# Kernel optimization log

Hardware: AMD Instinct MI355X
Metric: run time of the kernel (lower is better)

The kernel has to match this reference:

```python
import jax, jax.numpy as jnp
import numpy as np

BOS_ID = 0
EOS_ID = 1


def setup_inputs() -> dict:
    key = jax.random.key(0)
    ks = jax.random.split(key, 16)
    B, L, F = 64, 200, 512
    H, E, A = 512, 512, 512
    V, T = 50257, 21
    D = E + F  # rnn input_dim
    s = lambda n: 1.0 / np.sqrt(n)
    ref = jax.random.randint(ks[0], (B, T), 2, V, dtype=jnp.int32)
    ref = ref.at[:, 0].set(BOS_ID).at[:, -1].set(EOS_ID)
    return {
        "encoder_output": jax.random.normal(ks[1], (B, L, F), jnp.float32),
        "decoder_init_hidden": jax.random.normal(ks[2], (1, B, H), jnp.float32),
        "encoding_mask": jnp.ones((B, L, 1), jnp.float32),
        "temp_seg": jax.random.uniform(ks[3], (B, 2), jnp.float32),
        "embed_table": jax.random.normal(ks[4], (V, E), jnp.float32) * 0.02,
        "W_ih": jax.random.normal(ks[5], (3 * H, D), jnp.float32) * s(D),
        "W_hh": jax.random.normal(ks[6], (3 * H, H), jnp.float32) * s(H),
        "b_ih": jnp.zeros((3 * H,), jnp.float32),
        "b_hh": jnp.zeros((3 * H,), jnp.float32),
        "Wa_enc": jax.random.normal(ks[7], (F, A), jnp.float32) * s(F),
        "Wa_h": jax.random.normal(ks[8], (H, A), jnp.float32) * s(H),
        "v_att": jax.random.normal(ks[9], (A,), jnp.float32) * s(A),
        "W_out": jax.random.normal(ks[10], (V, H), jnp.float32) * s(H),
        "b_out": jnp.zeros((V,), jnp.float32),
        "ref_caption": ref,
    }


def reference(encoder_output, decoder_init_hidden, encoding_mask, temp_seg,
              embed_table, W_ih, W_hh, b_ih, b_hh,
              Wa_enc, Wa_h, v_att, W_out, b_out, ref_caption):
    # Teacher-forced training forward of RNNSeqDecoder (GRU, 1 layer).
    B, T = ref_caption.shape
    V = embed_table.shape[0]
    enc_proj = jnp.einsum('blf,fa->bla', encoder_output, Wa_enc)  # precompute attn enc term
    mask = encoding_mask[..., 0]  # (B,L)
    h0 = decoder_init_hidden[0]   # (B,H)

    def step(h, word):
        emb = embed_table[word]                                        # (B,E)
        # additive attention over encoder states (masked)
        score = jnp.einsum('bla,a->bl', jnp.tanh(enc_proj + (h @ Wa_h)[:, None, :]), v_att)
        score = jnp.where(mask > 0, score, -1e9)
        attn = jax.nn.softmax(score, axis=1)
        ctx = jnp.einsum('bl,blf->bf', attn, encoder_output)           # (B,F)
        x = jnp.concatenate([emb, ctx], axis=1)                        # (B,E+F)
        # PyTorch GRU cell
        gi = x @ W_ih.T + b_ih
        gh = h @ W_hh.T + b_hh
        i_r, i_z, i_n = jnp.split(gi, 3, axis=1)
        h_r, h_z, h_n = jnp.split(gh, 3, axis=1)
        r = jax.nn.sigmoid(i_r + h_r)
        z = jax.nn.sigmoid(i_z + h_z)
        n = jnp.tanh(i_n + r * h_n)
        h_new = (1.0 - z) * n + z * h
        logp = jax.nn.log_softmax(h_new @ W_out.T + b_out, axis=1)     # (B,V)
        return h_new, logp

    _, logps = jax.lax.scan(step, h0, ref_caption[:, :-1].T)           # (T-1,B,V)
    first = jnp.zeros((B, 1, V), logps.dtype)  # BOS_ID == 0, matches torch.zeros(...) + BOS_ID
    caption_prob = jnp.concatenate([first, jnp.swapaxes(logps, 0, 1)], axis=1)  # (B,T,V)
    return caption_prob
```

## Files before the change

kernel.cpp:

```cpp
#include <hip/hip_runtime.h>
#include <stdint.h>
#include <stddef.h>

#define B_ 64
#define L_ 200
#define F_ 512
#define H_ 512
#define A_ 512
#define E_ 512
#define V_ 50257
#define PADV 50304
#define T_ 21
#define D_ 1024
#define NBLK_LOG 786
#define BH (B_ * H_)
#define BD (B_ * D_)
#define NROW 1280

typedef __attribute__((ext_vector_type(8))) short short8;
typedef __attribute__((ext_vector_type(4))) float f32x4;

__device__ __forceinline__ unsigned short f2b(float f) {
  unsigned int u = __builtin_bit_cast(unsigned int, f);
  u += 0x7FFFu + ((u >> 16) & 1u);
  return (unsigned short)(u >> 16);
}
__device__ __forceinline__ float b2f(unsigned short s) {
  unsigned int u = ((unsigned int)s) << 16;
  return __builtin_bit_cast(float, u);
}
__device__ __forceinline__ f32x4 mfma16(short8 a, short8 b, f32x4 c) {
  return __builtin_amdgcn_mfma_f32_16x16x32_bf16(a, b, c, 0, 0, 0);
}
__device__ __forceinline__ int hsoff(int b, int j) {
  return (((b >> 4) * 16 + (j >> 5)) * 64 + (((j >> 3) & 3) * 16 + (b & 15))) * 8 + (j & 7);
}
__device__ __forceinline__ int xoff(int b, int k) {
  return (((b >> 4) * 32 + (k >> 5)) * 64 + (((k >> 3) & 3) * 16 + (b & 15))) * 8 + (k & 7);
}


__global__ void k_cvt(const float* __restrict__ src, unsigned short* __restrict__ dst, int n4) {
  int i = blockIdx.x * blockDim.x + threadIdx.x;
  int stride = gridDim.x * blockDim.x;
  const float4* s4 = (const float4*)src;
  ushort4* d4 = (ushort4*)dst;
  for (; i < n4; i += stride) {
    float4 v = s4[i];
    ushort4 o;
    o.x = f2b(v.x); o.y = f2b(v.y); o.z = f2b(v.z); o.w = f2b(v.w);
    d4[i] = o;
  }
}

__global__ void k_wfrag(const float* __restrict__ src, unsigned short* __restrict__ dst, int K) {
  int rt = blockIdx.x;
  int r15 = threadIdx.x & 15;
  int row = rt * 16 + r15;
  int nch = K >> 3;
  int kpw = K >> 5;
  for (int kc = threadIdx.x >> 4; kc < nch; kc += 16) {
    const float4* s = (const float4*)(src + (size_t)row * K + kc * 8);
    float4 x = s[0], y = s[1];
    short8 o;
    o[0] = f2b(x.x); o[1] = f2b(x.y); o[2] = f2b(x.z); o[3] = f2b(x.w);
    o[4] = f2b(y.x); o[5] = f2b(y.y); o[6] = f2b(y.z); o[7] = f2b(y.w);
    *(short8*)(dst + ((size_t)(rt * kpw + (kc >> 2)) * 64 + ((kc & 3) * 16 + r15)) * 8) = o;
  }
}

__global__ void k_transcvt(const float* __restrict__ src, unsigned short* __restrict__ dst, int R, int C) {
  __shared__ float tile[64][65];
  int cb = blockIdx.x * 64, rb = blockIdx.y * 64;
  int tx = threadIdx.x & 63, ty = threadIdx.x >> 6;
#pragma unroll
  for (int i = 0; i < 16; ++i) {
    int r = ty * 16 + i;
    tile[r][tx] = src[(size_t)(rb + r) * C + cb + tx];
  }
  __syncthreads();
#pragma unroll
  for (int i = 0; i < 16; ++i) {
    int c = ty * 16 + i;
    dst[(size_t)(cb + c) * R + rb + tx] = f2b(tile[tx][c]);
  }
}

__global__ void k_trans32(const float* __restrict__ src, float* __restrict__ dst, int R, int C) {
  __shared__ float tile[64][65];
  int cb = blockIdx.x * 64, rb = blockIdx.y * 64;
  int tx = threadIdx.x & 63, ty = threadIdx.x >> 6;
#pragma unroll
  for (int i = 0; i < 16; ++i) {
    int r = ty * 16 + i;
    tile[r][tx] = src[(size_t)(rb + r) * C + cb + tx];
  }
  __syncthreads();
#pragma unroll
  for (int i = 0; i < 16; ++i) {
    int c = ty * 16 + i;
    dst[(size_t)(cb + c) * R + rb + tx] = tile[tx][c];
  }
}

__global__ void k_hs0(const float* __restrict__ src, unsigned short* __restrict__ hs) {
  int b = blockIdx.x;
  for (int j = threadIdx.x; j < H_; j += 256)
    hs[hsoff(b, j)] = f2b(src[(size_t)b * H_ + j]);
}

__global__ void k_embAll(const int* __restrict__ ref, const float* __restrict__ et,
                         unsigned short* __restrict__ xAll) {
  int b = blockIdx.x, tp = blockIdx.y;
  int word = ref[b * T_ + tp];
  const float* er = et + (size_t)word * E_;
  unsigned short* dst = xAll + (size_t)tp * BD;
  int c = threadIdx.x;
  const float4* s = (const float4*)(er + c * 8);
  float4 x = s[0], y = s[1];
  short8 o;
  o[0] = f2b(x.x); o[1] = f2b(x.y); o[2] = f2b(x.z); o[3] = f2b(x.w);
  o[4] = f2b(y.x); o[5] = f2b(y.y); o[6] = f2b(y.z); o[7] = f2b(y.w);
  *(short8*)(dst + xoff(b, c * 8)) = o;
}

__global__ __launch_bounds__(256, 2) void k_encproj2(const unsigned short* __restrict__ encb,
                                                     const unsigned short* __restrict__ WaTb,
                                                     unsigned short* __restrict__ epb) {
  __shared__ unsigned short al[32768];
  int tid = threadIdx.x;
  size_t rowbase = (size_t)blockIdx.x * 64;
  for (int idx = tid; idx < 4096; idx += 256) {
    int row = idx >> 6, seg = idx & 63;
    unsigned char* dp = (unsigned char*)al + row * 1024 + ((seg * 16) ^ ((row & 7) << 4));
    *(short8*)dp = *(const short8*)(encb + (rowbase + row) * F_ + seg * 8);
  }
  __syncthreads();
  int w = tid >> 6, lane = tid & 63, ln15 = lane & 15, g = lane >> 4;
  int sw = (ln15 & 7) << 4;
  const unsigned char* alb = (const unsigned char*)al;
  int mrow = w * 16 + ln15;
  for (int nt = 0; nt < 32; ++nt) {
    f32x4 acc = {0.f, 0.f, 0.f, 0.f};
    const unsigned short* brow = WaTb + (size_t)(nt * 16 + ln15) * F_ + 8 * g;
#pragma unroll 4
    for (int kk = 0; kk < 16; ++kk) {
      short8 bf = *(const short8*)(brow + kk * 32);
      short8 af = *(const short8*)(alb + mrow * 1024 + ((kk * 64 + 16 * g) ^ sw));
      acc = mfma16(af, bf, acc);
    }
#pragma unroll
    for (int r = 0; r < 4; ++r) {
      size_t m = rowbase + w * 16 + 4 * g + r;
      epb[m * A_ + nt * 16 + ln15] = f2b(acc[r]);
    }
  }
}

__global__ void k_zero0(float* __restrict__ out) {
  int b = blockIdx.y;
  float* o = out + (size_t)b * T_ * V_;
  int v0 = blockIdx.x * 1024 + threadIdx.x;
#pragma unroll
  for (int i = 0; i < 4; ++i) { int v = v0 + i * 256; if (v < V_) o[v] = 0.f; }
}


__global__ __launch_bounds__(256) void k_hwgh(const unsigned short* __restrict__ Wahf,
                                              const unsigned short* __restrict__ Wfhh,
                                              const unsigned short* __restrict__ hs,
                                              float* __restrict__ hw,
                                              float* __restrict__ ghG) {
  int blk = blockIdx.x;
  int w = threadIdx.x >> 6, lane = threadIdx.x & 63;
  int ln15 = lane & 15, g = lane >> 4;
  if (blk < 32) {
    f32x4 acc = {0.f, 0.f, 0.f, 0.f};
#pragma unroll 4
    for (int kk = 0; kk < 16; ++kk) {
      short8 av = *(const short8*)(Wahf + (((size_t)blk * 16 + kk) * 64 + lane) * 8);
      short8 hv = *(const short8*)(hs + (((size_t)w * 16 + kk) * 64 + lane) * 8);
      acc = mfma16(av, hv, acc);
    }
#pragma unroll
    for (int r = 0; r < 4; ++r) {
      int a = blk * 16 + 4 * g + r;
      int b = w * 16 + ln15;
      hw[(size_t)b * 512 + a] = acc[r];
    }
  } else {
    int base = (blk - 32) * 3;
#pragma unroll
    for (int i = 0; i < 3; ++i) {
      int jt = base + i;
      f32x4 acc = {0.f, 0.f, 0.f, 0.f};
#pragma unroll
      for (int kk = 0; kk < 16; ++kk) {
        short8 wv = *(const short8*)(Wfhh + (((size_t)jt * 16 + kk) * 64 + lane) * 8);
        short8 hv = *(const short8*)(hs + (((size_t)w * 16 + kk) * 64 + lane) * 8);
        acc = mfma16(wv, hv, acc);
      }
#pragma unroll
      for (int r = 0; r < 4; ++r) {
        int j = jt * 16 + 4 * g + r;
        int b = w * 16 + ln15;
        ghG[(size_t)j * B_ + b] = acc[r];
      }
    }
  }
}


__global__ __launch_bounds__(1024) void k_attB(const float* __restrict__ mask,
                                               const float* __restrict__ vatt,
                                               const unsigned short* __restrict__ encb,
                                               const unsigned short* __restrict__ epb,
                                               const float* __restrict__ hw,
                                               unsigned short* __restrict__ xplane) {
  __shared__ float sm[208];
  __shared__ float ctxp[16][F_];
  __shared__ float ctxF[F_];
  int b = blockIdx.x;
  int tid = threadIdx.x;
  int w = tid >> 6, lane = tid & 63;
  float hwv[8], vv[8];
  {
    const float4* hp = (const float4*)(hw + (size_t)b * 512 + lane * 8);
    const float4* vp = (const float4*)(vatt + lane * 8);
    float4 h0 = hp[0], h1 = hp[1], v0 = vp[0], v1 = vp[1];
    hwv[0] = h0.x; hwv[1] = h0.y; hwv[2] = h0.z; hwv[3] = h0.w;
    hwv[4] = h1.x; hwv[5] = h1.y; hwv[6] = h1.z; hwv[7] = h1.w;
    vv[0] = v0.x; vv[1] = v0.y; vv[2] = v0.z; vv[3] = v0.w;
    vv[4] = v1.x; vv[5] = v1.y; vv[6] = v1.z; vv[7] = v1.w;
  }
  for (int l = w; l < L_; l += 16) {
    short8 ev = *(const short8*)(epb + ((size_t)(b * L_ + l)) * 512 + lane * 8);
    float p = 0.f;
#pragma unroll
    for (int j = 0; j < 8; ++j) {
      float x = b2f((unsigned short)ev[j]) + hwv[j];
      float e2 = __expf(x + x);
      p = fmaf(1.f - 2.f / (e2 + 1.f), vv[j], p);
    }
    for (int o = 1; o < 64; o <<= 1) p += __shfl_xor(p, o);
    if (lane == 0) {
      float mk = mask[b * L_ + l];
      sm[l] = (mk > 0.f) ? p : -1e9f;
    }
  }
  __syncthreads();
  if (tid < 64) {
    float m = -1e30f;
    for (int l = tid; l < L_; l += 64) m = fmaxf(m, sm[l]);
    for (int o = 1; o < 64; o <<= 1) m = fmaxf(m, __shfl_xor(m, o));
    float s = 0.f;
    for (int l = tid; l < L_; l += 64) s += __expf(sm[l] - m);
    for (int o = 1; o < 64; o <<= 1) s += __shfl_xor(s, o);
    float inv = 1.f / s;
    for (int l = tid; l < L_; l += 64) sm[l] = __expf(sm[l] - m) * inv;
  }
  __syncthreads();
  float c[8] = {0.f, 0.f, 0.f, 0.f, 0.f, 0.f, 0.f, 0.f};
  for (int l = w; l < L_; l += 16) {
    float wgt = sm[l];
    short8 ev = *(const short8*)(encb + ((size_t)(b * L_ + l)) * 512 + lane * 8);
#pragma unroll
    for (int j = 0; j < 8; ++j) c[j] = fmaf(wgt, b2f((unsigned short)ev[j]), c[j]);
  }
#pragma unroll
  for (int j = 0; j < 8; ++j) ctxp[w][lane * 8 + j] = c[j];
  __syncthreads();
  if (tid < 512) {
    float s = 0.f;
#pragma unroll
    for (int q = 0; q < 16; ++q) s += ctxp[q][tid];
    ctxF[tid] = s;
  }
  __syncthreads();
  if (tid < 64) {
    short8 o;
#pragma unroll
    for (int j = 0; j < 8; ++j) o[j] = f2b(ctxF[tid * 8 + j]);
    *(short8*)(xplane + xoff(b, E_ + tid * 8)) = o;
  }
}


__global__ __launch_bounds__(256) void k_stepB(const unsigned short* __restrict__ Wfih,
                                               const float* __restrict__ bih,
                                               const float* __restrict__ bhh,
                                               const unsigned short* __restrict__ xplane,
                                               const float* __restrict__ ghG,
                                               const float* __restrict__ hBold,
                                               unsigned short* __restrict__ hsnew,
                                               float* __restrict__ hBnew) {
  int bx = blockIdx.x;
  int w = threadIdx.x >> 6, lane = threadIdx.x & 63;
  int ln15 = lane & 15, g = lane >> 4;
  f32x4 z4 = {0.f, 0.f, 0.f, 0.f};
  f32x4 aIr = z4, aIz = z4, aIn = z4;
#pragma unroll 2
  for (int kk = 0; kk < 32; ++kk) {
    short8 xv = *(const short8*)(xplane + (((size_t)w * 32 + kk) * 64 + lane) * 8);
    aIr = mfma16(*(const short8*)(Wfih + (((size_t)(0 * 32 + bx) * 32 + kk) * 64 + lane) * 8), xv, aIr);
    aIz = mfma16(*(const short8*)(Wfih + (((size_t)(32 + bx) * 32 + kk) * 64 + lane) * 8), xv, aIz);
    aIn = mfma16(*(const short8*)(Wfih + (((size_t)(64 + bx) * 32 + kk) * 64 + lane) * 8), xv, aIn);
  }
  int jb = bx * 16;
#pragma unroll
  for (int r = 0; r < 4; ++r) {
    int j = jb + 4 * g + r;
    int b = w * 16 + ln15;
    float ir = aIr[r] + bih[j];
    float iz = aIz[r] + bih[512 + j];
    float in_ = aIn[r] + bih[1024 + j];
    float hrv = ghG[(size_t)j * B_ + b] + bhh[j];
    float hzv = ghG[(size_t)(512 + j) * B_ + b] + bhh[512 + j];
    float hnv = ghG[(size_t)(1024 + j) * B_ + b] + bhh[1024 + j];
    float rg = 1.f / (1.f + __expf(-(ir + hrv)));
    float zg = 1.f / (1.f + __expf(-(iz + hzv)));
    float e2 = __expf(2.f * (in_ + rg * hnv));
    float ng = 1.f - 2.f / (e2 + 1.f);
    float ho = hBold[(size_t)b * H_ + j];
    float hv = (1.f - zg) * ng + zg * ho;
    hBnew[(size_t)b * H_ + j] = hv;
    hsnew[hsoff(b, j)] = f2b(hv);
  }
}


__global__ __launch_bounds__(256) void k_blog(const unsigned short* __restrict__ Wb,
                                              const float* __restrict__ bout,
                                              const unsigned short* __restrict__ hsAll,
                                              float* __restrict__ out,
                                              unsigned short* __restrict__ lws, int mode) {
  __shared__ float tile[2][64][68];
  int tid = threadIdx.x;
  int w = tid >> 6, lane = tid & 63, ln15 = lane & 15, g = lane >> 4;
  int vcol = blockIdx.x * 64 + w * 16 + ln15;
  bool vok = vcol < V_;
  int vr = vok ? vcol : (V_ - 1);
  const unsigned short* brow = Wb + (size_t)vr * H_ + 8 * g;
  short8 wb[16];
#pragma unroll
  for (int kk = 0; kk < 16; ++kk) wb[kk] = *(const short8*)(brow + kk * 32);
  float bo = bout[vr];
  int row = tid >> 2, seg = tid & 3;

  for (int t = 0; t < T_ - 1; ++t) {
    const unsigned short* hp = hsAll + (size_t)(t + 1) * BH;
    int buf = t & 1;
#pragma unroll
    for (int mp = 0; mp < 2; ++mp) {
      f32x4 z4 = {0.f, 0.f, 0.f, 0.f};
      f32x4 acc0 = z4, acc1 = z4;
#pragma unroll
      for (int kk = 0; kk < 16; ++kk) {
        short8 a0 = *(const short8*)(hp + (((mp * 2 + 0) * 16 + kk) * 64 + lane) * 8);
        short8 a1 = *(const short8*)(hp + (((mp * 2 + 1) * 16 + kk) * 64 + lane) * 8);
        acc0 = mfma16(a0, wb[kk], acc0);
        acc1 = mfma16(a1, wb[kk], acc1);
      }
#pragma unroll
      for (int r = 0; r < 4; ++r) {
        int bi0 = (mp * 2 + 0) * 16 + 4 * g + r;
        int bi1 = (mp * 2 + 1) * 16 + 4 * g + r;
        tile[buf][bi0][w * 16 + ln15] = vok ? acc0[r] + bo : -1e30f;
        tile[buf][bi1][w * 16 + ln15] = vok ? acc1[r] + bo : -1e30f;
      }
    }
    __syncthreads();
    float v[16];
#pragma unroll
    for (int q = 0; q < 4; ++q) {
      float4 fv = *(const float4*)&tile[buf][row][seg * 16 + q * 4];
      v[q * 4 + 0] = fv.x; v[q * 4 + 1] = fv.y; v[q * 4 + 2] = fv.z; v[q * 4 + 3] = fv.w;
    }
    int cb = blockIdx.x * 64 + seg * 16;
    if (mode == 1) {
      unsigned short* orow = lws + ((size_t)t * 64 + row) * PADV + cb;
      short8 o0, o1;
#pragma unroll
      for (int i = 0; i < 8; ++i) { o0[i] = f2b(v[i]); o1[i] = f2b(v[8 + i]); }
      *(short8*)orow = o0;
      *(short8*)(orow + 8) = o1;
    } else {
      float* orow = out + ((size_t)row * T_ + (t + 1)) * V_ + cb;
      if (cb + 16 <= V_) {
#pragma unroll
        for (int q = 0; q < 4; ++q)
          *(float4*)(orow + q * 4) = make_float4(v[q * 4], v[q * 4 + 1], v[q * 4 + 2], v[q * 4 + 3]);
      } else {
        for (int i = 0; i < 16; ++i)
          if (cb + i < V_) orow[i] = v[i];
      }
    }
  }
}

__global__ __launch_bounds__(256) void k_lsefin(const unsigned short* __restrict__ lws,
                                                float* __restrict__ out) {
  __shared__ float lm[256], ls[256];
  __shared__ float lvs;
  int rho = blockIdx.x;
  int tp = rho >> 6, b = rho & 63;
  const unsigned short* src = lws + (size_t)(tp * 64 + b) * PADV;
  float* o = out + ((size_t)b * T_ + (tp + 1)) * V_;
  int tid = threadIdx.x;
  float m = -1e30f, s = 0.f;
  for (int i = tid; i < PADV / 8; i += 256) {
    short8 sv = *(const short8*)(src + i * 8);
    float x0 = b2f((unsigned short)sv[0]), x1 = b2f((unsigned short)sv[1]);
    float x2 = b2f((unsigned short)sv[2]), x3 = b2f((unsigned short)sv[3]);
    float x4 = b2f((unsigned short)sv[4]), x5 = b2f((unsigned short)sv[5]);
    float x6 = b2f((unsigned short)sv[6]), x7 = b2f((unsigned short)sv[7]);
    float cm = fmaxf(fmaxf(fmaxf(x0, x1), fmaxf(x2, x3)), fmaxf(fmaxf(x4, x5), fmaxf(x6, x7)));
    float cs = __expf(x0 - cm) + __expf(x1 - cm) + __expf(x2 - cm) + __expf(x3 - cm) +
               __expf(x4 - cm) + __expf(x5 - cm) + __expf(x6 - cm) + __expf(x7 - cm);
    float nm = fmaxf(m, cm);
    s = s * __expf(m - nm) + cs * __expf(cm - nm);
    m = nm;
  }
  lm[tid] = m; ls[tid] = s;
  __syncthreads();
  for (int o2 = 128; o2 > 0; o2 >>= 1) {
    if (tid < o2) {
      float m2 = lm[tid + o2], s2 = ls[tid + o2];
      float nm = fmaxf(lm[tid], m2);
      ls[tid] = ls[tid] * __expf(lm[tid] - nm) + s2 * __expf(m2 - nm);
      lm[tid] = nm;
    }
    __syncthreads();
  }
  if (tid == 0) lvs = lm[0] + logf(ls[0]);
  __syncthreads();
  float Lv = lvs;
  for (int i = tid; i < 6282; i += 256) {
    short8 sv = *(const short8*)(src + i * 8);
    float4 v0, v1;
    v0.x = b2f((unsigned short)sv[0]) - Lv; v0.y = b2f((unsigned short)sv[1]) - Lv;
    v0.z = b2f((unsigned short)sv[2]) - Lv; v0.w = b2f((unsigned short)sv[3]) - Lv;
    v1.x = b2f((unsigned short)sv[4]) - Lv; v1.y = b2f((unsigned short)sv[5]) - Lv;
    v1.z = b2f((unsigned short)sv[6]) - Lv; v1.w = b2f((unsigned short)sv[7]) - Lv;
    *(float4*)(o + i * 8) = v0;
    *(float4*)(o + i * 8 + 4) = v1;
  }
  if (tid == 0) o[50256] = b2f(src[50256]) - Lv;
}

__global__ __launch_bounds__(256) void k_lsefin0(float* __restrict__ out) {
  __shared__ float lm[256], ls[256];
  __shared__ float lvs;
  int rho = blockIdx.x;
  int tp = rho >> 6, b = rho & 63;
  float* o = out + ((size_t)b * T_ + (tp + 1)) * V_;
  int tid = threadIdx.x;
  float m = -1e30f, s = 0.f;
  for (int v = tid; v < V_; v += 256) {
    float x = o[v];
    float nm = fmaxf(m, x);
    s = s * __expf(m - nm) + __expf(x - nm);
    m = nm;
  }
  lm[tid] = m; ls[tid] = s;
  __syncthreads();
  for (int o2 = 128; o2 > 0; o2 >>= 1) {
    if (tid < o2) {
      float m2 = lm[tid + o2], s2 = ls[tid + o2];
      float nm = fmaxf(lm[tid], m2);
      ls[tid] = ls[tid] * __expf(lm[tid] - nm) + s2 * __expf(m2 - nm);
      lm[tid] = nm;
    }
    __syncthreads();
  }
  if (tid == 0) lvs = lm[0] + logf(ls[0]);
  __syncthreads();
  float Lv = lvs;
  for (int v = tid; v < V_; v += 256) o[v] -= Lv;
}


extern "C" void kernel_launch(void* const* d_in, const int* in_sizes, int n_in,
                              void* d_out, int out_size, void* d_ws, size_t ws_size,
                              hipStream_t stream) {
  const float* enc   = (const float*)d_in[0];
  const float* dih   = (const float*)d_in[1];
  const float* mask  = (const float*)d_in[2];
  const float* et    = (const float*)d_in[4];
  const float* Wih   = (const float*)d_in[5];
  const float* Whh   = (const float*)d_in[6];
  const float* bih   = (const float*)d_in[7];
  const float* bhh   = (const float*)d_in[8];
  const float* Waenc = (const float*)d_in[9];
  const float* Wah   = (const float*)d_in[10];
  const float* vatt  = (const float*)d_in[11];
  const float* Wout  = (const float*)d_in[12];
  const float* bout  = (const float*)d_in[13];
  const int*   ref   = (const int*)d_in[14];
  float* out = (float*)d_out;

  char* w = (char*)d_ws;
  size_t o = 0;
  unsigned short* Wb    = (unsigned short*)(w + o); o += (size_t)V_ * H_ * 2;
  unsigned short* Wfih  = (unsigned short*)(w + o); o += (size_t)1536 * 1024 * 2;
  unsigned short* Wfhh  = (unsigned short*)(w + o); o += (size_t)1536 * 512 * 2;
  unsigned short* WaTb  = (unsigned short*)(w + o); o += (size_t)512 * 512 * 2;
  unsigned short* Wahf  = (unsigned short*)(w + o); o += (size_t)512 * 512 * 2;
  float* WahT32 = (float*)(w + o); o += (size_t)512 * 512 * 4;
  unsigned short* encb  = (unsigned short*)(w + o); o += (size_t)B_ * L_ * F_ * 2;
  unsigned short* epb   = (unsigned short*)(w + o); o += (size_t)B_ * L_ * A_ * 2;
  unsigned short* xAll  = (unsigned short*)(w + o); o += (size_t)20 * BD * 2;
  unsigned short* hsAll = (unsigned short*)(w + o); o += (size_t)T_ * BH * 2;
  float* hBAll = (float*)(w + o); o += (size_t)T_ * BH * 4;
  float* ghG   = (float*)(w + o); o += (size_t)1536 * B_ * 4;
  float* hw    = (float*)(w + o); o += (size_t)B_ * A_ * 4 + 256;
  unsigned short* lws = (unsigned short*)(w + o);
  size_t need = o + (size_t)NROW * PADV * 2;
  int mode = (ws_size >= need) ? 1 : 0;

  k_cvt<<<4096, 256, 0, stream>>>(Wout, Wb, V_ * H_ / 4);
  k_cvt<<<2048, 256, 0, stream>>>(enc, encb, B_ * L_ * F_ / 4);
  k_wfrag<<<96, 256, 0, stream>>>(Wih, Wfih, 1024);
  k_wfrag<<<96, 256, 0, stream>>>(Whh, Wfhh, 512);
  k_transcvt<<<dim3(8, 8), 256, 0, stream>>>(Waenc, WaTb, 512, 512);
  k_trans32<<<dim3(8, 8), 256, 0, stream>>>(Wah, WahT32, 512, 512);
  k_wfrag<<<32, 256, 0, stream>>>(WahT32, Wahf, 512);
  k_hs0<<<64, 256, 0, stream>>>(dih, hsAll);
  k_embAll<<<dim3(64, 20), 64, 0, stream>>>(ref, et, xAll);
  k_encproj2<<<200, 256, 0, stream>>>(encb, WaTb, epb);
  k_zero0<<<dim3(50, 64), 256, 0, stream>>>(out);

  for (int t = 0; t < T_ - 1; ++t) {
    const float* hB_t = (t == 0) ? dih : (hBAll + (size_t)t * BH);
    float* hB_n = hBAll + (size_t)(t + 1) * BH;
    const unsigned short* hs_t = hsAll + (size_t)t * BH;
    unsigned short* hs_n = hsAll + (size_t)(t + 1) * BH;
    unsigned short* xp = xAll + (size_t)t * BD;
    k_hwgh<<<64, 256, 0, stream>>>(Wahf, Wfhh, hs_t, hw, ghG);
    k_attB<<<64, 1024, 0, stream>>>(mask, vatt, encb, epb, hw, xp);
    k_stepB<<<32, 256, 0, stream>>>(Wfih, bih, bhh, xp, ghG, hB_t, hs_n, hB_n);
  }
  k_blog<<<NBLK_LOG, 256, 0, stream>>>(Wb, bout, hsAll, out, lws, mode);
  if (mode == 1) k_lsefin<<<1280, 256, 0, stream>>>(lws, out);
  else k_lsefin0<<<1280, 256, 0, stream>>>(out);
}
```

Baseline: 1.362 ms.

## Fuse t=0 zeroing into log-softmax finalize, cache row in LDS, raise MFMA priority

The separate kernel that zeroes the BOS time slice is removed. Those 64 rows are now zeroed by 64 extra blocks appended to the log-softmax finalize launch, which saves one kernel launch. The bf16 finalize kernel now runs with 512 threads and keeps each logit row in a ~100KB LDS buffer during the max/sum pass, so the normalize pass reads from LDS instead of re-reading global memory. The large LDS footprint limits occupancy to about one block per CU. The logits GEMM also raises wave priority with s_setprio around its MFMA section.

```diff
diff --git a/kernel.cpp b/kernel.cpp
--- a/kernel.cpp
+++ b/kernel.cpp
@@ -155,14 +155,6 @@
       epb[m * A_ + nt * 16 + ln15] = f2b(acc[r]);
     }
   }
-}
-
-__global__ void k_zero0(float* __restrict__ out) {
-  int b = blockIdx.y;
-  float* o = out + (size_t)b * T_ * V_;
-  int v0 = blockIdx.x * 1024 + threadIdx.x;
-#pragma unroll
-  for (int i = 0; i < 4; ++i) { int v = v0 + i * 256; if (v < V_) o[v] = 0.f; }
 }
 
 
@@ -350,6 +342,7 @@
   for (int t = 0; t < T_ - 1; ++t) {
     const unsigned short* hp = hsAll + (size_t)(t + 1) * BH;
     int buf = t & 1;
+    __builtin_amdgcn_s_setprio(1);
 #pragma unroll
     for (int mp = 0; mp < 2; ++mp) {
       f32x4 z4 = {0.f, 0.f, 0.f, 0.f};
@@ -369,6 +362,7 @@
         tile[buf][bi1][w * 16 + ln15] = vok ? acc1[r] + bo : -1e30f;
       }
     }
+    __builtin_amdgcn_s_setprio(0);
     __syncthreads();
     float v[16];
 #pragma unroll
@@ -398,18 +392,29 @@
   }
 }
 
-__global__ __launch_bounds__(256) void k_lsefin(const unsigned short* __restrict__ lws,
+__global__ __launch_bounds__(512) void k_lsefin(const unsigned short* __restrict__ lws,
                                                 float* __restrict__ out) {
-  __shared__ float lm[256], ls[256];
+  __shared__ unsigned short srow[PADV];
+  __shared__ float lm[512], ls[512];
   __shared__ float lvs;
-  int rho = blockIdx.x;
+  int bid = blockIdx.x;
+  int tid = threadIdx.x;
+  if (bid >= NROW) {
+    int b = bid - NROW;
+    float* o = out + (size_t)b * T_ * V_;
+    float4 z = make_float4(0.f, 0.f, 0.f, 0.f);
+    for (int i = tid; i < 12564; i += 512) *(float4*)(o + i * 4) = z;
+    if (tid == 0) o[50256] = 0.f;
+    return;
+  }
+  int rho = bid;
   int tp = rho >> 6, b = rho & 63;
   const unsigned short* src = lws + (size_t)(tp * 64 + b) * PADV;
   float* o = out + ((size_t)b * T_ + (tp + 1)) * V_;
-  int tid = threadIdx.x;
   float m = -1e30f, s = 0.f;
-  for (int i = tid; i < PADV / 8; i += 256) {
+  for (int i = tid; i < PADV / 8; i += 512) {
     short8 sv = *(const short8*)(src + i * 8);
+    *(short8*)(srow + i * 8) = sv;
     float x0 = b2f((unsigned short)sv[0]), x1 = b2f((unsigned short)sv[1]);
     float x2 = b2f((unsigned short)sv[2]), x3 = b2f((unsigned short)sv[3]);
     float x4 = b2f((unsigned short)sv[4]), x5 = b2f((unsigned short)sv[5]);
@@ -423,7 +428,7 @@
   }
   lm[tid] = m; ls[tid] = s;
   __syncthreads();
-  for (int o2 = 128; o2 > 0; o2 >>= 1) {
+  for (int o2 = 256; o2 > 0; o2 >>= 1) {
     if (tid < o2) {
       float m2 = lm[tid + o2], s2 = ls[tid + o2];
       float nm = fmaxf(lm[tid], m2);
@@ -435,8 +440,8 @@
   if (tid == 0) lvs = lm[0] + logf(ls[0]);
   __syncthreads();
   float Lv = lvs;
-  for (int i = tid; i < 6282; i += 256) {
-    short8 sv = *(const short8*)(src + i * 8);
+  for (int i = tid; i < 6282; i += 512) {
+    short8 sv = *(const short8*)(srow + i * 8);
     float4 v0, v1;
     v0.x = b2f((unsigned short)sv[0]) - Lv; v0.y = b2f((unsigned short)sv[1]) - Lv;
     v0.z = b2f((unsigned short)sv[2]) - Lv; v0.w = b2f((unsigned short)sv[3]) - Lv;
@@ -445,16 +450,23 @@
     *(float4*)(o + i * 8) = v0;
     *(float4*)(o + i * 8 + 4) = v1;
   }
-  if (tid == 0) o[50256] = b2f(src[50256]) - Lv;
+  if (tid == 0) o[50256] = b2f(srow[50256]) - Lv;
 }
 
 __global__ __launch_bounds__(256) void k_lsefin0(float* __restrict__ out) {
   __shared__ float lm[256], ls[256];
   __shared__ float lvs;
-  int rho = blockIdx.x;
+  int bid = blockIdx.x;
+  int tid = threadIdx.x;
+  if (bid >= NROW) {
+    int b = bid - NROW;
+    float* o = out + (size_t)b * T_ * V_;
+    for (int v = tid; v < V_; v += 256) o[v] = 0.f;
+    return;
+  }
+  int rho = bid;
   int tp = rho >> 6, b = rho & 63;
   float* o = out + ((size_t)b * T_ + (tp + 1)) * V_;
-  int tid = threadIdx.x;
   float m = -1e30f, s = 0.f;
   for (int v = tid; v < V_; v += 256) {
     float x = o[v];
@@ -528,7 +540,6 @@
   k_hs0<<<64, 256, 0, stream>>>(dih, hsAll);
   k_embAll<<<dim3(64, 20), 64, 0, stream>>>(ref, et, xAll);
   k_encproj2<<<200, 256, 0, stream>>>(encb, WaTb, epb);
-  k_zero0<<<dim3(50, 64), 256, 0, stream>>>(out);
 
   for (int t = 0; t < T_ - 1; ++t) {
     const float* hB_t = (t == 0) ? dih : (hBAll + (size_t)t * BH);
@@ -541,6 +552,6 @@
     k_stepB<<<32, 256, 0, stream>>>(Wfih, bih, bhh, xp, ghG, hB_t, hs_n, hB_n);
   }
   k_blog<<<NBLK_LOG, 256, 0, stream>>>(Wb, bout, hsAll, out, lws, mode);
-  if (mode == 1) k_lsefin<<<1280, 256, 0, stream>>>(lws, out);
-  else k_lsefin0<<<1280, 256, 0, stream>>>(out);
-}
+  if (mode == 1) k_lsefin<<<NROW + 64, 512, 0, stream>>>(lws, out);
+  else k_lsefin0<<<NROW + 64, 256, 0, stream>>>(out);
+}
```

Measured after the change: 1.356 ms. About the same (-0.5%).
